# Kernel tuning notes

Measured on AMD Instinct MI355X. Metric: run time of the kernel, lower is better.

## Reference

```python
import jax, jax.numpy as jnp
import numpy as np


def ternarize_weight(w):
    # abs-mean threshold quantization to {-am, 0, +am}
    abs_mean = jnp.maximum(jnp.abs(w).mean(), 1e-5)
    thr = 0.7 * abs_mean
    q = jnp.where(w > thr, 1.0, jnp.where(w < -thr, -1.0, 0.0))
    # STE: forward value is q*abs_mean, grad flows to w as identity
    return w + jax.lax.stop_gradient(q * abs_mean - w)


def rotate_half(x):
    x1, x2 = jnp.split(x, 2, axis=-1)
    return jnp.concatenate([-x2, x1], axis=-1)


def setup_inputs() -> dict:
    key = jax.random.key(0)
    k1, k2, k3, k4, k5 = jax.random.split(key, 5)
    B, T, C, H = 2, 2048, 1024, 16
    D = C // H
    x = jax.random.normal(k1, (B, T, C), dtype=jnp.float32)
    cos = jax.random.uniform(k2, (1, 1, T, D), dtype=jnp.float32)
    sin = jax.random.uniform(k3, (1, 1, T, D), dtype=jnp.float32)
    w_qkv = jax.random.normal(k4, (3 * C, C), dtype=jnp.float32) / np.sqrt(C)
    w_proj = jax.random.normal(k5, (C, C), dtype=jnp.float32) / np.sqrt(C)
    return {"x": x, "cos": cos, "sin": sin, "w_qkv": w_qkv, "w_proj": w_proj}


def reference(x, cos, sin, w_qkv, w_proj):
    B, T, C = x.shape
    H = 16
    D = C // H
    wq = ternarize_weight(w_qkv)
    wp = ternarize_weight(w_proj)
    qkv = x @ wq.T  # [B,T,3C]
    q, k, v = jnp.split(qkv, 3, axis=-1)
    # [B,T,C] -> [B,H,T,D]
    q = q.reshape(B, T, H, D).transpose(0, 2, 1, 3)
    k = k.reshape(B, T, H, D).transpose(0, 2, 1, 3)
    v = v.reshape(B, T, H, D).transpose(0, 2, 1, 3)
    # RoPE
    q = q * cos + rotate_half(q) * sin
    k = k * cos + rotate_half(k) * sin
    # causal SDPA
    scale = 1.0 / np.sqrt(D)
    scores = jnp.einsum("bhqd,bhkd->bhqk", q, k) * scale
    causal = jnp.tril(jnp.ones((T, T), dtype=bool))
    scores = jnp.where(causal, scores, jnp.finfo(scores.dtype).min)
    attn = jax.nn.softmax(scores, axis=-1)
    y = jnp.einsum("bhqk,bhkd->bhqd", attn, v)  # [B,H,T,D]
    y = y.transpose(0, 2, 1, 3).reshape(B, T, C)
    return y @ wp.T
```

## Files before the change

kernel.cpp:

```cpp
#include <hip/hip_runtime.h>
#include <hip/hip_bf16.h>

#define B_ 2
#define T_ 2048
#define C_ 1024
#define H_ 16
#define D_ 64
#define M_ 4096
#define N3C 3072

using short8  = __attribute__((ext_vector_type(8))) short;
using floatx4 = __attribute__((ext_vector_type(4))) float;
typedef unsigned int u32;

__device__ __forceinline__ unsigned short f2b(float f) {
  __hip_bfloat16 h = __float2bfloat16(f);
  return *reinterpret_cast<unsigned short*>(&h);
}
__device__ __forceinline__ float b2f(unsigned short u) {
  union { unsigned int i; float f; } x; x.i = ((unsigned int)u) << 16; return x.f;
}
__device__ __forceinline__ u32 pk2(float a, float b) {
  float2 t; t.x = a; t.y = b;
  __hip_bfloat162 p = __float22bfloat162_rn(t);
  return *reinterpret_cast<u32*>(&p);
}

__device__ __forceinline__ void gll16(const void* g, void* l) {
  __builtin_amdgcn_global_load_lds((const __attribute__((address_space(1))) u32*)g,
                                   (__attribute__((address_space(3))) u32*)l, 16, 0, 0);
}

#define SYNCV(N) do {                                                   \
    asm volatile("s_waitcnt vmcnt(" #N ")" ::: "memory");               \
    __builtin_amdgcn_s_barrier();                                       \
    asm volatile("" ::: "memory");                                      \
  } while (0)


__global__ void abs_sum2(const float* __restrict__ wq, const float* __restrict__ wp,
                         double* __restrict__ sums) {
  __shared__ double red[4];
  const float* w = blockIdx.y ? wp : wq;
  const int n4 = blockIdx.y ? (C_ * C_ / 4) : (3 * C_ * C_ / 4);
  int stride = gridDim.x * blockDim.x;
  double s = 0.0;
  for (int i = blockIdx.x * blockDim.x + threadIdx.x; i < n4; i += stride) {
    float4 v = ((const float4*)w)[i];
    s += (double)fabsf(v.x) + (double)fabsf(v.y) + (double)fabsf(v.z) + (double)fabsf(v.w);
  }
  #pragma unroll
  for (int off = 32; off > 0; off >>= 1)
    s += __shfl_down(s, off, 64);
  if ((threadIdx.x & 63) == 0) red[threadIdx.x >> 6] = s;
  __syncthreads();
  if (threadIdx.x == 0) atomicAdd(sums + blockIdx.y, (red[0] + red[1]) + (red[2] + red[3]));
}

__global__ void tern_cvt(const float* __restrict__ wq, const float* __restrict__ wp,
                         const float* __restrict__ x,
                         unsigned short* __restrict__ oq, unsigned short* __restrict__ op,
                         unsigned short* __restrict__ xb,
                         const double* __restrict__ sums, float* __restrict__ ams) {
  const int NQ = 3 * C_ * C_;
  const int NP = C_ * C_;
  int i = blockIdx.x * blockDim.x + threadIdx.x;
  float am0 = fmaxf((float)(sums[0] * (1.0 / NQ)), 1e-5f);
  float am1 = fmaxf((float)(sums[1] * (1.0 / NP)), 1e-5f);
  if (i == 0) { ams[0] = am0; ams[1] = am1; }
  if (i < NQ) {
    float thr = 0.7f * am0, v = wq[i];
    oq[i] = (v > thr) ? 0x3F80u : ((v < -thr) ? 0xBF80u : 0u);
  } else if (i < NQ + NP) {
    int j = i - NQ;
    float thr = 0.7f * am1, v = wp[j];
    op[j] = (v > thr) ? 0x3F80u : ((v < -thr) ? 0xBF80u : 0u);
  } else {
    int j = i - NQ - NP;
    float4 v = ((const float4*)x)[j];
    ushort4 o; o.x = f2b(v.x); o.y = f2b(v.y); o.z = f2b(v.z); o.w = f2b(v.w);
    ((ushort4*)xb)[j] = o;
  }
}


__global__ __launch_bounds__(256) void gemm_qkv(const unsigned short* __restrict__ A,
                                                const unsigned short* __restrict__ W,
                                                const float* __restrict__ scale_ptr,
                                                const float* __restrict__ cosp,
                                                const float* __restrict__ sinp,
                                                unsigned short* __restrict__ Qb,
                                                unsigned short* __restrict__ Kb,
                                                unsigned short* __restrict__ Vtb) {
  const int K = C_;
  __shared__ __attribute__((aligned(16))) unsigned short As[3][128 * 32];
  __shared__ __attribute__((aligned(16))) unsigned short Ws[3][192 * 32];
  const int tid = threadIdx.x, lane = tid & 63, wv = tid >> 6;
  const int m = lane & 15, g = lane >> 4;
  const int m0 = blockIdx.y * 128, n0 = blockIdx.x * 192;
  const int wm = (wv >> 1) * 64, wn = wv & 1;

  const int srow16 = lane >> 2;
  const int skoff = (lane & 3) * 8;
  const unsigned short* ga0 = A + (size_t)(m0 + wv * 32 + srow16) * K + skoff;
  const unsigned short* ga1 = A + (size_t)(m0 + wv * 32 + 16 + srow16) * K + skoff;
  const unsigned short* gw0 = W + (size_t)(n0 + (wv + 0) * 16 + srow16) * K + skoff;
  const unsigned short* gw1 = W + (size_t)(n0 + (wv + 4) * 16 + srow16) * K + skoff;
  const unsigned short* gw2 = W + (size_t)(n0 + (wv + 8) * 16 + srow16) * K + skoff;
  const int oA0 = (wv * 32) * 32;
  const int oA1 = (wv * 32 + 16) * 32;
  const int oW0 = ((wv + 0) * 16) * 32;
  const int oW1 = ((wv + 4) * 16) * 32;
  const int oW2 = ((wv + 8) * 16) * 32;

  floatx4 acc[4][6] = {};

#define QSTAGE(T) do {                                                    \
    gll16(ga0, &As[T][oA0]); gll16(ga1, &As[T][oA1]);                     \
    gll16(gw0, &Ws[T][oW0]); gll16(gw1, &Ws[T][oW1]);                     \
    gll16(gw2, &Ws[T][oW2]);                                              \
    ga0 += 32; ga1 += 32; gw0 += 32; gw1 += 32; gw2 += 32;                \
  } while (0)

#define QCOMP(T) do {                                                     \
    short8 af[4], wf[6];                                                  \
    _Pragma("unroll")                                                     \
    for (int r = 0; r < 4; r++)                                           \
      af[r] = *(const short8*)&As[T][(wm + r * 16 + m) * 32 + g * 8];     \
    _Pragma("unroll")                                                     \
    for (int j = 0; j < 6; j++)                                           \
      wf[j] = *(const short8*)&Ws[T][((2 * j + wn) * 16 + m) * 32 + g * 8]; \
    _Pragma("unroll")                                                     \
    for (int r = 0; r < 4; r++)                                           \
      _Pragma("unroll")                                                   \
      for (int j = 0; j < 6; j++)                                         \
        acc[r][j] = __builtin_amdgcn_mfma_f32_16x16x32_bf16(af[r], wf[j], acc[r][j], 0, 0, 0); \
  } while (0)

  QSTAGE(0);
  QSTAGE(1);
  SYNCV(5);
  for (int tt = 0; tt < 10; ++tt) {
    QSTAGE(2); QCOMP(0); SYNCV(5);
    QSTAGE(0); QCOMP(1); SYNCV(5);
    QSTAGE(1); QCOMP(2); SYNCV(5);
  }
  QCOMP(0); SYNCV(0);
  QCOMP(1);
#undef QSTAGE
#undef QCOMP

  const float am = *scale_ptr;
  #pragma unroll
  for (int j = 0; j < 6; j++) {
    const int colb = n0 + (2 * j + wn) * 16;
    const int sect = colb >> 10;
    const int h = (colb >> 6) & 15;
    const int pb = colb & 63;
    const int p = pb + m;
    if (sect < 2) {
      unsigned short* dst = sect ? Kb : Qb;
      const float sc = sect ? am : am * 0.18033688011112042f;
      const bool hi = (pb & 32) != 0;
      #pragma unroll
      for (int r = 0; r < 4; r++)
        #pragma unroll
        for (int i = 0; i < 4; i++) {
          int row = m0 + wm + r * 16 + g * 4 + i;
          int t = row & (T_ - 1), b = row >> 11;
          float cv = cosp[t * 64 + p], sv = sinp[t * 64 + p];
          float a = acc[r][j][i], pt = acc[r][j ^ 1][i];
          float val = hi ? (a * cv + pt * sv) : (a * cv - pt * sv);
          dst[((size_t)(b * H_ + h) * T_ + t) * 64 + p] = f2b(val * sc);
        }
    } else {
      #pragma unroll
      for (int r = 0; r < 4; r++)
        #pragma unroll
        for (int i = 0; i < 4; i++) {
          int row = m0 + wm + r * 16 + g * 4 + i;
          int t = row & (T_ - 1), b = row >> 11;
          size_t hbase = (size_t)(b * H_ + h) * 64 * T_;
          Vtb[hbase + (size_t)p * T_ + t] = f2b(acc[r][j][i] * am);
        }
    }
  }
}


__global__ __launch_bounds__(256) void gemm_proj(const unsigned short* __restrict__ A,
                                                 const unsigned short* __restrict__ W,
                                                 const float* __restrict__ scale_ptr,
                                                 float* __restrict__ Cout) {
  const int K = C_, N = C_;
  __shared__ __attribute__((aligned(16))) unsigned short As[3][128 * 32];
  __shared__ __attribute__((aligned(16))) unsigned short Ws[3][128 * 32];
  const int tid = threadIdx.x, lane = tid & 63, wv = tid >> 6;
  const int m = lane & 15, g = lane >> 4;
  const int m0 = blockIdx.y * 128, n0 = blockIdx.x * 128;
  const int wm = (wv >> 1) * 64, wn = (wv & 1) * 64;

  const int srow16 = lane >> 2;
  const int skoff = (lane & 3) * 8;
  const unsigned short* ga0 = A + (size_t)(m0 + wv * 32 + srow16) * K + skoff;
  const unsigned short* ga1 = A + (size_t)(m0 + wv * 32 + 16 + srow16) * K + skoff;
  const unsigned short* gw0 = W + (size_t)(n0 + wv * 32 + srow16) * K + skoff;
  const unsigned short* gw1 = W + (size_t)(n0 + wv * 32 + 16 + srow16) * K + skoff;
  const int o0 = (wv * 32) * 32;
  const int o1 = (wv * 32 + 16) * 32;

  floatx4 acc[4][4] = {};

#define PSTAGE(T) do {                                                    \
    gll16(ga0, &As[T][o0]); gll16(ga1, &As[T][o1]);                       \
    gll16(gw0, &Ws[T][o0]); gll16(gw1, &Ws[T][o1]);                       \
    ga0 += 32; ga1 += 32; gw0 += 32; gw1 += 32;                           \
  } while (0)

#define PCOMP(T) do {                                                     \
    short8 af[4], wf[4];                                                  \
    _Pragma("unroll")                                                     \
    for (int r = 0; r < 4; r++)                                           \
      af[r] = *(const short8*)&As[T][(wm + r * 16 + m) * 32 + g * 8];     \
    _Pragma("unroll")                                                     \
    for (int c = 0; c < 4; c++)                                           \
      wf[c] = *(const short8*)&Ws[T][(wn + c * 16 + m) * 32 + g * 8];     \
    _Pragma("unroll")                                                     \
    for (int r = 0; r < 4; r++)                                           \
      _Pragma("unroll")                                                   \
      for (int c = 0; c < 4; c++)                                         \
        acc[r][c] = __builtin_amdgcn_mfma_f32_16x16x32_bf16(af[r], wf[c], acc[r][c], 0, 0, 0); \
  } while (0)

  PSTAGE(0);
  PSTAGE(1);
  SYNCV(4);
  for (int tt = 0; tt < 10; ++tt) {
    PSTAGE(2); PCOMP(0); SYNCV(4);
    PSTAGE(0); PCOMP(1); SYNCV(4);
    PSTAGE(1); PCOMP(2); SYNCV(4);
  }
  PCOMP(0); SYNCV(0);
  PCOMP(1);
#undef PSTAGE
#undef PCOMP

  const float scale = *scale_ptr;
  #pragma unroll
  for (int r = 0; r < 4; r++)
    #pragma unroll
    for (int c = 0; c < 4; c++)
      #pragma unroll
      for (int i = 0; i < 4; i++) {
        int row = m0 + wm + r * 16 + g * 4 + i;
        int col = n0 + wn + c * 16 + m;
        Cout[(size_t)row * N + col] = acc[r][c][i] * scale;
      }
}


__global__ __launch_bounds__(256) void flash_mfma(const unsigned short* __restrict__ Qb,
                                                  const unsigned short* __restrict__ Kb,
                                                  const unsigned short* __restrict__ Vtb,
                                                  unsigned short* __restrict__ Y) {
  __shared__ __align__(16) unsigned short Ktile[2][64][64];
  __shared__ __align__(16) unsigned short Vtile[2][64][64];
  __shared__ __align__(16) unsigned short Plds[4][16][72];
  const int lane = threadIdx.x & 63;
  const int wv = threadIdx.x >> 6;
  const int m = lane & 15, g = lane >> 4;
  const int gid = blockIdx.x;
  const int xcd = gid & 7, j = gid >> 3;
  const int bh = xcd * 4 + (j & 3);
  const int s = 31 - (j >> 2);
  const int b = bh >> 4, h = bh & 15;
  const size_t hb = (size_t)bh * T_ * 64;
  const unsigned short* Kbh = Kb + hb;
  const unsigned short* Vbh = Vtb + hb;
  const int r8 = lane >> 3, cc8 = lane & 7;
  const int gcol = ((cc8 ^ r8) << 3);

  const int ntiles = s + 1;
  const int qbase = s * 64 + wv * 16;
  const int q_glob = qbase + m;

  const unsigned short* qp = Qb + hb + (size_t)(qbase + m) * 64 + g * 8;
  short8 qf0 = *(const short8*)qp;
  short8 qf1 = *(const short8*)(qp + 32);

  short8 ones;
  #pragma unroll
  for (int i = 0; i < 8; i++) ones[i] = (short)0x3F80;

  floatx4 O[4] = {};
  floatx4 accl = {};

  #pragma unroll
  for (int cc = 0; cc < 2; cc++) {
    int row = wv * 16 + cc * 8;
    gll16(Kbh + (size_t)(row + r8) * 64 + gcol, &Ktile[0][row][0]);
    gll16(Vbh + (size_t)(row + r8) * T_ + gcol, &Vtile[0][row][0]);
  }

  for (int kt = 0; kt < ntiles; kt++) {
    const int buf = kt & 1;
    const int kb = kt * 64;
    __syncthreads();
    if (kt + 1 < ntiles) {
      const int kb2 = kb + 64;
      #pragma unroll
      for (int cc = 0; cc < 2; cc++) {
        int row = wv * 16 + cc * 8;
        gll16(Kbh + (size_t)(kb2 + row + r8) * 64 + gcol, &Ktile[1 - buf][row][0]);
        gll16(Vbh + (size_t)(row + r8) * T_ + kb2 + gcol, &Vtile[1 - buf][row][0]);
      }
    }
    floatx4 S[4];
    #pragma unroll
    for (int mt = 0; mt < 4; mt++) {
      int row = mt * 16 + m;
      short8 kf0 = *(const short8*)&Ktile[buf][row][(g ^ (m & 7)) << 3];
      short8 kf1 = *(const short8*)&Ktile[buf][row][((g + 4) ^ (m & 7)) << 3];
      floatx4 sv = {};
      sv = __builtin_amdgcn_mfma_f32_16x16x32_bf16(kf0, qf0, sv, 0, 0, 0);
      sv = __builtin_amdgcn_mfma_f32_16x16x32_bf16(kf1, qf1, sv, 0, 0, 0);
      S[mt] = sv;
    }
    if (kt + 1 < ntiles) {
      #pragma unroll
      for (int mt = 0; mt < 4; mt++) {
        uint2 w;
        w.x = pk2(exp2f(S[mt][0]), exp2f(S[mt][1]));
        w.y = pk2(exp2f(S[mt][2]), exp2f(S[mt][3]));
        *(uint2*)&Plds[wv][m][mt * 16 + g * 4] = w;
      }
    } else {
      #pragma unroll
      for (int mt = 0; mt < 4; mt++) {
        float e[4];
        #pragma unroll
        for (int r = 0; r < 4; r++) {
          int kg = kb + mt * 16 + g * 4 + r;
          e[r] = (kg <= q_glob) ? exp2f(S[mt][r]) : 0.f;
        }
        uint2 w;
        w.x = pk2(e[0], e[1]);
        w.y = pk2(e[2], e[3]);
        *(uint2*)&Plds[wv][m][mt * 16 + g * 4] = w;
      }
    }
    short8 pa0 = *(const short8*)&Plds[wv][m][g * 8];
    short8 pa1 = *(const short8*)&Plds[wv][m][32 + g * 8];
    #pragma unroll
    for (int nt = 0; nt < 4; nt++) {
      int row = nt * 16 + m;
      short8 v0 = *(const short8*)&Vtile[buf][row][(g ^ (m & 7)) << 3];
      short8 v1 = *(const short8*)&Vtile[buf][row][((g + 4) ^ (m & 7)) << 3];
      O[nt] = __builtin_amdgcn_mfma_f32_16x16x32_bf16(pa0, v0, O[nt], 0, 0, 0);
      O[nt] = __builtin_amdgcn_mfma_f32_16x16x32_bf16(pa1, v1, O[nt], 0, 0, 0);
    }
    accl = __builtin_amdgcn_mfma_f32_16x16x32_bf16(pa0, ones, accl, 0, 0, 0);
    accl = __builtin_amdgcn_mfma_f32_16x16x32_bf16(pa1, ones, accl, 0, 0, 0);
  }

  float li[4];
  #pragma unroll
  for (int r = 0; r < 4; r++) li[r] = 1.0f / accl[r];
  #pragma unroll
  for (int nt = 0; nt < 4; nt++)
    #pragma unroll
    for (int r = 0; r < 4; r++) {
      int trow = qbase + g * 4 + r;
      int col = h * 64 + nt * 16 + m;
      Y[(size_t)(b * T_ + trow) * C_ + col] = f2b(O[nt][r] * li[r]);
    }
}


extern "C" void kernel_launch(void* const* d_in, const int* in_sizes, int n_in,
                              void* d_out, int out_size, void* d_ws, size_t ws_size,
                              hipStream_t stream) {
  (void)in_sizes; (void)n_in; (void)out_size; (void)ws_size;
  const float* x      = (const float*)d_in[0];
  const float* cosp   = (const float*)d_in[1];
  const float* sinp   = (const float*)d_in[2];
  const float* w_qkv  = (const float*)d_in[3];
  const float* w_proj = (const float*)d_in[4];
  float* out = (float*)d_out;

  char* ws = (char*)d_ws;
  double* sums = (double*)ws;
  float*  ams  = (float*)(ws + 16);
  unsigned short* wqkv_b  = (unsigned short*)(ws + 256);
  unsigned short* wproj_b = wqkv_b + (size_t)N3C * C_;
  unsigned short* xb      = wproj_b + (size_t)C_ * C_;
  unsigned short* Qb      = xb + (size_t)M_ * C_;
  unsigned short* Kb      = Qb + (size_t)B_ * H_ * T_ * D_;
  unsigned short* Vtb     = Kb + (size_t)B_ * H_ * T_ * D_;
  unsigned short* yb      = Vtb + (size_t)B_ * H_ * T_ * D_;

  hipMemsetAsync(sums, 0, 16, stream);
  abs_sum2<<<dim3(256, 2), 256, 0, stream>>>(w_qkv, w_proj, sums);
  tern_cvt<<<(4 * C_ * C_ + M_ * C_ / 4) / 256, 256, 0, stream>>>(w_qkv, w_proj, x,
                                                                  wqkv_b, wproj_b, xb,
                                                                  sums, ams);
  gemm_qkv<<<dim3(N3C / 192, M_ / 128), 256, 0, stream>>>(xb, wqkv_b, ams + 0,
                                                          cosp, sinp, Qb, Kb, Vtb);
  flash_mfma<<<1024, 256, 0, stream>>>(Qb, Kb, Vtb, yb);
  gemm_proj<<<dim3(C_ / 128, M_ / 128), 256, 0, stream>>>(yb, wproj_b, ams + 1, out);
}
```

Measured before the change: 198.0 us.

## Process 128-query blocks per workgroup with triple-buffered K/V tiles and priority hints

Each workgroup now handles 128 query rows, with each wave owning two 16-row groups, so every K/V tile loaded into LDS is reused twice as much and the grid is halved. K/V staging moves from double to triple buffering with a partial vmcnt wait (SYNCV) instead of a full barrier per tile. s_setprio is raised around the MFMA blocks. Causal skipping is done per wave (kt <= t_d). The trade-off is more registers and LDS per block and fewer blocks, which can reduce occupancy and worsen load balance across the causal triangle.

```diff
diff --git a/kernel.cpp b/kernel.cpp
--- a/kernel.cpp
+++ b/kernel.cpp
@@ -263,117 +263,152 @@
                                                   const unsigned short* __restrict__ Kb,
                                                   const unsigned short* __restrict__ Vtb,
                                                   unsigned short* __restrict__ Y) {
-  __shared__ __align__(16) unsigned short Ktile[2][64][64];
-  __shared__ __align__(16) unsigned short Vtile[2][64][64];
-  __shared__ __align__(16) unsigned short Plds[4][16][72];
+  __shared__ __align__(16) unsigned short KT[3 * 64 * 64];
+  __shared__ __align__(16) unsigned short VT[3 * 64 * 64];
+  __shared__ __align__(16) unsigned short Plds[4][2][16][72];
   const int lane = threadIdx.x & 63;
   const int wv = threadIdx.x >> 6;
   const int m = lane & 15, g = lane >> 4;
   const int gid = blockIdx.x;
   const int xcd = gid & 7, j = gid >> 3;
   const int bh = xcd * 4 + (j & 3);
-  const int s = 31 - (j >> 2);
+  const int qb = 15 - (j >> 2);
   const int b = bh >> 4, h = bh & 15;
   const size_t hb = (size_t)bh * T_ * 64;
-  const unsigned short* Kbh = Kb + hb;
-  const unsigned short* Vbh = Vtb + hb;
   const int r8 = lane >> 3, cc8 = lane & 7;
   const int gcol = ((cc8 ^ r8) << 3);
 
-  const int ntiles = s + 1;
-  const int qbase = s * 64 + wv * 16;
-  const int q_glob = qbase + m;
-
-  const unsigned short* qp = Qb + hb + (size_t)(qbase + m) * 64 + g * 8;
-  short8 qf0 = *(const short8*)qp;
-  short8 qf1 = *(const short8*)(qp + 32);
+  const int ntiles = 2 * qb + 2;
+  const int q0 = qb * 128 + wv * 32;
+  const int t_d = q0 >> 6;
+
+  short8 qf[2][2];
+  #pragma unroll
+  for (int qg = 0; qg < 2; qg++) {
+    const unsigned short* qp = Qb + hb + (size_t)(q0 + qg * 16 + m) * 64 + g * 8;
+    qf[qg][0] = *(const short8*)qp;
+    qf[qg][1] = *(const short8*)(qp + 32);
+  }
+
+  const unsigned short* kp = Kb + hb + (size_t)(wv * 16 + r8) * 64 + gcol;
+  const unsigned short* vp = Vtb + hb + (size_t)(wv * 16 + r8) * T_ + gcol;
 
   short8 ones;
   #pragma unroll
   for (int i = 0; i < 8; i++) ones[i] = (short)0x3F80;
 
-  floatx4 O[4] = {};
-  floatx4 accl = {};
-
-  #pragma unroll
-  for (int cc = 0; cc < 2; cc++) {
-    int row = wv * 16 + cc * 8;
-    gll16(Kbh + (size_t)(row + r8) * 64 + gcol, &Ktile[0][row][0]);
-    gll16(Vbh + (size_t)(row + r8) * T_ + gcol, &Vtile[0][row][0]);
+  floatx4 O[4][2] = {};
+  floatx4 accl[2] = {};
+
+  int curo = 0, nxto = 4096, thdo = 8192;
+
+  {
+    const int dst = (wv * 16) * 64;
+    gll16(kp,          &KT[dst]);
+    gll16(kp + 8 * 64, &KT[dst + 8 * 64]);
+    gll16(vp,          &VT[dst]);
+    gll16(vp + 8 * T_, &VT[dst + 8 * 64]);
+    kp += 64 * 64; vp += 64;
   }
 
   for (int kt = 0; kt < ntiles; kt++) {
-    const int buf = kt & 1;
-    const int kb = kt * 64;
-    __syncthreads();
     if (kt + 1 < ntiles) {
-      const int kb2 = kb + 64;
-      #pragma unroll
-      for (int cc = 0; cc < 2; cc++) {
-        int row = wv * 16 + cc * 8;
-        gll16(Kbh + (size_t)(kb2 + row + r8) * 64 + gcol, &Ktile[1 - buf][row][0]);
-        gll16(Vbh + (size_t)(row + r8) * T_ + kb2 + gcol, &Vtile[1 - buf][row][0]);
-      }
+      const int dst = nxto + (wv * 16) * 64;
+      gll16(kp,          &KT[dst]);
+      gll16(kp + 8 * 64, &KT[dst + 8 * 64]);
+      gll16(vp,          &VT[dst]);
+      gll16(vp + 8 * T_, &VT[dst + 8 * 64]);
+      kp += 64 * 64; vp += 64;
+      SYNCV(4);
+    } else {
+      SYNCV(0);
     }
-    floatx4 S[4];
+    if (kt <= t_d) {
+      floatx4 S[4][2] = {};
+      __builtin_amdgcn_s_setprio(1);
+      #pragma unroll
+      for (int mt = 0; mt < 4; mt++) {
+        const int row = curo + (mt * 16 + m) * 64;
+        short8 kf0 = *(const short8*)&KT[row + ((g ^ (m & 7)) << 3)];
+        short8 kf1 = *(const short8*)&KT[row + (((g + 4) ^ (m & 7)) << 3)];
+        #pragma unroll
+        for (int qg = 0; qg < 2; qg++) {
+          S[mt][qg] = __builtin_amdgcn_mfma_f32_16x16x32_bf16(kf0, qf[qg][0], S[mt][qg], 0, 0, 0);
+          S[mt][qg] = __builtin_amdgcn_mfma_f32_16x16x32_bf16(kf1, qf[qg][1], S[mt][qg], 0, 0, 0);
+        }
+      }
+      __builtin_amdgcn_s_setprio(0);
+      if (kt < t_d) {
+        #pragma unroll
+        for (int qg = 0; qg < 2; qg++)
+          #pragma unroll
+          for (int mt = 0; mt < 4; mt++) {
+            uint2 w;
+            w.x = pk2(exp2f(S[mt][qg][0]), exp2f(S[mt][qg][1]));
+            w.y = pk2(exp2f(S[mt][qg][2]), exp2f(S[mt][qg][3]));
+            *(uint2*)&Plds[wv][qg][m][mt * 16 + g * 4] = w;
+          }
+      } else {
+        #pragma unroll
+        for (int qg = 0; qg < 2; qg++) {
+          const int qglob = q0 + qg * 16 + m;
+          #pragma unroll
+          for (int mt = 0; mt < 4; mt++) {
+            float e[4];
+            #pragma unroll
+            for (int r = 0; r < 4; r++) {
+              int kg = kt * 64 + mt * 16 + g * 4 + r;
+              e[r] = (kg <= qglob) ? exp2f(S[mt][qg][r]) : 0.f;
+            }
+            uint2 w;
+            w.x = pk2(e[0], e[1]);
+            w.y = pk2(e[2], e[3]);
+            *(uint2*)&Plds[wv][qg][m][mt * 16 + g * 4] = w;
+          }
+        }
+      }
+      short8 pa[2][2];
+      #pragma unroll
+      for (int qg = 0; qg < 2; qg++) {
+        pa[qg][0] = *(const short8*)&Plds[wv][qg][m][g * 8];
+        pa[qg][1] = *(const short8*)&Plds[wv][qg][m][32 + g * 8];
+      }
+      __builtin_amdgcn_s_setprio(1);
+      #pragma unroll
+      for (int nt = 0; nt < 4; nt++) {
+        const int row = curo + (nt * 16 + m) * 64;
+        short8 v0 = *(const short8*)&VT[row + ((g ^ (m & 7)) << 3)];
+        short8 v1 = *(const short8*)&VT[row + (((g + 4) ^ (m & 7)) << 3)];
+        #pragma unroll
+        for (int qg = 0; qg < 2; qg++) {
+          O[nt][qg] = __builtin_amdgcn_mfma_f32_16x16x32_bf16(pa[qg][0], v0, O[nt][qg], 0, 0, 0);
+          O[nt][qg] = __builtin_amdgcn_mfma_f32_16x16x32_bf16(pa[qg][1], v1, O[nt][qg], 0, 0, 0);
+        }
+      }
+      #pragma unroll
+      for (int qg = 0; qg < 2; qg++) {
+        accl[qg] = __builtin_amdgcn_mfma_f32_16x16x32_bf16(pa[qg][0], ones, accl[qg], 0, 0, 0);
+        accl[qg] = __builtin_amdgcn_mfma_f32_16x16x32_bf16(pa[qg][1], ones, accl[qg], 0, 0, 0);
+      }
+      __builtin_amdgcn_s_setprio(0);
+    }
+    int tmpo = curo; curo = nxto; nxto = thdo; thdo = tmpo;
+  }
+
+  #pragma unroll
+  for (int qg = 0; qg < 2; qg++) {
+    float li[4];
     #pragma unroll
-    for (int mt = 0; mt < 4; mt++) {
-      int row = mt * 16 + m;
-      short8 kf0 = *(const short8*)&Ktile[buf][row][(g ^ (m & 7)) << 3];
-      short8 kf1 = *(const short8*)&Ktile[buf][row][((g + 4) ^ (m & 7)) << 3];
-      floatx4 sv = {};
-      sv = __builtin_amdgcn_mfma_f32_16x16x32_bf16(kf0, qf0, sv, 0, 0, 0);
-      sv = __builtin_amdgcn_mfma_f32_16x16x32_bf16(kf1, qf1, sv, 0, 0, 0);
-      S[mt] = sv;
-    }
-    if (kt + 1 < ntiles) {
-      #pragma unroll
-      for (int mt = 0; mt < 4; mt++) {
-        uint2 w;
-        w.x = pk2(exp2f(S[mt][0]), exp2f(S[mt][1]));
-        w.y = pk2(exp2f(S[mt][2]), exp2f(S[mt][3]));
-        *(uint2*)&Plds[wv][m][mt * 16 + g * 4] = w;
-      }
-    } else {
-      #pragma unroll
-      for (int mt = 0; mt < 4; mt++) {
-        float e[4];
-        #pragma unroll
-        for (int r = 0; r < 4; r++) {
-          int kg = kb + mt * 16 + g * 4 + r;
-          e[r] = (kg <= q_glob) ? exp2f(S[mt][r]) : 0.f;
-        }
-        uint2 w;
-        w.x = pk2(e[0], e[1]);
-        w.y = pk2(e[2], e[3]);
-        *(uint2*)&Plds[wv][m][mt * 16 + g * 4] = w;
-      }
-    }
-    short8 pa0 = *(const short8*)&Plds[wv][m][g * 8];
-    short8 pa1 = *(const short8*)&Plds[wv][m][32 + g * 8];
+    for (int r = 0; r < 4; r++) li[r] = 1.0f / accl[qg][r];
     #pragma unroll
-    for (int nt = 0; nt < 4; nt++) {
-      int row = nt * 16 + m;
-      short8 v0 = *(const short8*)&Vtile[buf][row][(g ^ (m & 7)) << 3];
-      short8 v1 = *(const short8*)&Vtile[buf][row][((g + 4) ^ (m & 7)) << 3];
-      O[nt] = __builtin_amdgcn_mfma_f32_16x16x32_bf16(pa0, v0, O[nt], 0, 0, 0);
-      O[nt] = __builtin_amdgcn_mfma_f32_16x16x32_bf16(pa1, v1, O[nt], 0, 0, 0);
-    }
-    accl = __builtin_amdgcn_mfma_f32_16x16x32_bf16(pa0, ones, accl, 0, 0, 0);
-    accl = __builtin_amdgcn_mfma_f32_16x16x32_bf16(pa1, ones, accl, 0, 0, 0);
-  }
-
-  float li[4];
-  #pragma unroll
-  for (int r = 0; r < 4; r++) li[r] = 1.0f / accl[r];
-  #pragma unroll
-  for (int nt = 0; nt < 4; nt++)
-    #pragma unroll
-    for (int r = 0; r < 4; r++) {
-      int trow = qbase + g * 4 + r;
-      int col = h * 64 + nt * 16 + m;
-      Y[(size_t)(b * T_ + trow) * C_ + col] = f2b(O[nt][r] * li[r]);
-    }
+    for (int nt = 0; nt < 4; nt++)
+      #pragma unroll
+      for (int r = 0; r < 4; r++) {
+        int trow = q0 + qg * 16 + g * 4 + r;
+        int col = h * 64 + nt * 16 + m;
+        Y[(size_t)(b * T_ + trow) * C_ + col] = f2b(O[nt][qg][r] * li[r]);
+      }
+  }
 }
 
 
@@ -406,6 +441,6 @@
                                                                   sums, ams);
   gemm_qkv<<<dim3(N3C / 192, M_ / 128), 256, 0, stream>>>(xb, wqkv_b, ams + 0,
                                                           cosp, sinp, Qb, Kb, Vtb);
-  flash_mfma<<<1024, 256, 0, stream>>>(Qb, Kb, Vtb, yb);
+  flash_mfma<<<512, 256, 0, stream>>>(Qb, Kb, Vtb, yb);
   gemm_proj<<<dim3(C_ / 128, M_ / 128), 256, 0, stream>>>(yb, wproj_b, ams + 1, out);
 }
```

New measurement: 212.2 us. 7.1% more time.

## Load K/V fragments directly from global into registers in flash attention

Applied to the files above, without the earlier changes.

Drops the double-buffered LDS staging of K and V tiles and the per-iteration block barrier. Each wave now loads its own K and V MFMA fragments straight from global memory into registers, and the MFMA sections are wrapped in s_setprio raises. This removes the __syncthreads and LDS traffic, but the four waves in a block now each fetch the same K/V tile from global/L2, and no load is issued ahead of use to hide latency.

```diff
diff --git a/kernel.cpp b/kernel.cpp
--- a/kernel.cpp
+++ b/kernel.cpp
@@ -263,8 +263,6 @@
                                                   const unsigned short* __restrict__ Kb,
                                                   const unsigned short* __restrict__ Vtb,
                                                   unsigned short* __restrict__ Y) {
-  __shared__ __align__(16) unsigned short Ktile[2][64][64];
-  __shared__ __align__(16) unsigned short Vtile[2][64][64];
   __shared__ __align__(16) unsigned short Plds[4][16][72];
   const int lane = threadIdx.x & 63;
   const int wv = threadIdx.x >> 6;
@@ -275,10 +273,6 @@
   const int s = 31 - (j >> 2);
   const int b = bh >> 4, h = bh & 15;
   const size_t hb = (size_t)bh * T_ * 64;
-  const unsigned short* Kbh = Kb + hb;
-  const unsigned short* Vbh = Vtb + hb;
-  const int r8 = lane >> 3, cc8 = lane & 7;
-  const int gcol = ((cc8 ^ r8) << 3);
 
   const int ntiles = s + 1;
   const int qbase = s * 64 + wv * 16;
@@ -288,6 +282,9 @@
   short8 qf0 = *(const short8*)qp;
   short8 qf1 = *(const short8*)(qp + 32);
 
+  const unsigned short* kp = Kb + hb + m * 64 + g * 8;
+  const unsigned short* vp = Vtb + hb + (size_t)m * T_ + g * 8;
+
   short8 ones;
   #pragma unroll
   for (int i = 0; i < 8; i++) ones[i] = (short)0x3F80;
@@ -295,37 +292,30 @@
   floatx4 O[4] = {};
   floatx4 accl = {};
 
-  #pragma unroll
-  for (int cc = 0; cc < 2; cc++) {
-    int row = wv * 16 + cc * 8;
-    gll16(Kbh + (size_t)(row + r8) * 64 + gcol, &Ktile[0][row][0]);
-    gll16(Vbh + (size_t)(row + r8) * T_ + gcol, &Vtile[0][row][0]);
-  }
-
   for (int kt = 0; kt < ntiles; kt++) {
-    const int buf = kt & 1;
-    const int kb = kt * 64;
-    __syncthreads();
-    if (kt + 1 < ntiles) {
-      const int kb2 = kb + 64;
-      #pragma unroll
-      for (int cc = 0; cc < 2; cc++) {
-        int row = wv * 16 + cc * 8;
-        gll16(Kbh + (size_t)(kb2 + row + r8) * 64 + gcol, &Ktile[1 - buf][row][0]);
-        gll16(Vbh + (size_t)(row + r8) * T_ + kb2 + gcol, &Vtile[1 - buf][row][0]);
-      }
+    const unsigned short* kb_ = kp + (size_t)kt * 64 * 64;
+    const unsigned short* vb_ = vp + kt * 64;
+    short8 kf[4][2], vf[4][2];
+    #pragma unroll
+    for (int mt = 0; mt < 4; mt++) {
+      kf[mt][0] = *(const short8*)(kb_ + mt * 16 * 64);
+      kf[mt][1] = *(const short8*)(kb_ + mt * 16 * 64 + 32);
+    }
+    #pragma unroll
+    for (int nt = 0; nt < 4; nt++) {
+      vf[nt][0] = *(const short8*)(vb_ + (size_t)nt * 16 * T_);
+      vf[nt][1] = *(const short8*)(vb_ + (size_t)nt * 16 * T_ + 32);
     }
     floatx4 S[4];
+    __builtin_amdgcn_s_setprio(1);
     #pragma unroll
     for (int mt = 0; mt < 4; mt++) {
-      int row = mt * 16 + m;
-      short8 kf0 = *(const short8*)&Ktile[buf][row][(g ^ (m & 7)) << 3];
-      short8 kf1 = *(const short8*)&Ktile[buf][row][((g + 4) ^ (m & 7)) << 3];
       floatx4 sv = {};
-      sv = __builtin_amdgcn_mfma_f32_16x16x32_bf16(kf0, qf0, sv, 0, 0, 0);
-      sv = __builtin_amdgcn_mfma_f32_16x16x32_bf16(kf1, qf1, sv, 0, 0, 0);
+      sv = __builtin_amdgcn_mfma_f32_16x16x32_bf16(kf[mt][0], qf0, sv, 0, 0, 0);
+      sv = __builtin_amdgcn_mfma_f32_16x16x32_bf16(kf[mt][1], qf1, sv, 0, 0, 0);
       S[mt] = sv;
     }
+    __builtin_amdgcn_s_setprio(0);
     if (kt + 1 < ntiles) {
       #pragma unroll
       for (int mt = 0; mt < 4; mt++) {
@@ -340,7 +330,7 @@
         float e[4];
         #pragma unroll
         for (int r = 0; r < 4; r++) {
-          int kg = kb + mt * 16 + g * 4 + r;
+          int kg = kt * 64 + mt * 16 + g * 4 + r;
           e[r] = (kg <= q_glob) ? exp2f(S[mt][r]) : 0.f;
         }
         uint2 w;
@@ -351,16 +341,15 @@
     }
     short8 pa0 = *(const short8*)&Plds[wv][m][g * 8];
     short8 pa1 = *(const short8*)&Plds[wv][m][32 + g * 8];
+    __builtin_amdgcn_s_setprio(1);
     #pragma unroll
     for (int nt = 0; nt < 4; nt++) {
-      int row = nt * 16 + m;
-      short8 v0 = *(const short8*)&Vtile[buf][row][(g ^ (m & 7)) << 3];
-      short8 v1 = *(const short8*)&Vtile[buf][row][((g + 4) ^ (m & 7)) << 3];
-      O[nt] = __builtin_amdgcn_mfma_f32_16x16x32_bf16(pa0, v0, O[nt], 0, 0, 0);
-      O[nt] = __builtin_amdgcn_mfma_f32_16x16x32_bf16(pa1, v1, O[nt], 0, 0, 0);
+      O[nt] = __builtin_amdgcn_mfma_f32_16x16x32_bf16(pa0, vf[nt][0], O[nt], 0, 0, 0);
+      O[nt] = __builtin_amdgcn_mfma_f32_16x16x32_bf16(pa1, vf[nt][1], O[nt], 0, 0, 0);
     }
     accl = __builtin_amdgcn_mfma_f32_16x16x32_bf16(pa0, ones, accl, 0, 0, 0);
     accl = __builtin_amdgcn_mfma_f32_16x16x32_bf16(pa1, ones, accl, 0, 0, 0);
+    __builtin_amdgcn_s_setprio(0);
   }
 
   float li[4];
```

Result: slower. 287.8 us (+45.3%).
